# Optimization experiments

Measured on AMD Instinct MI355X. Metric: run time of the kernel, lower is better.

The kernel has to match this reference:

```python
import jax, jax.numpy as jnp
import numpy as np

G, N, C_IN, C_OUT, HEADS = 64, 2048, 64, 64, 2
E = 1_000_000
T = G * N  # total flattened nodes
NEG_SLOPE = 0.2  # PyG GATv2Conv default


def setup_inputs() -> dict:
    key = jax.random.key(0)
    k_x, k_e, k_wl, k_wr, k_a, k_b = jax.random.split(key, 6)
    x = jax.random.normal(k_x, (G, N, C_IN), dtype=jnp.float32)
    edge_index = jax.random.randint(k_e, (2, E), 0, T, dtype=jnp.int64)
    # GATv2Conv params (share_weights=False): separate lin_l / lin_r, per-head att vector, bias
    s = 1.0 / np.sqrt(C_IN)
    W_l = jax.random.uniform(k_wl, (C_IN, HEADS * C_OUT), minval=-s, maxval=s, dtype=jnp.float32)
    W_r = jax.random.uniform(k_wr, (C_IN, HEADS * C_OUT), minval=-s, maxval=s, dtype=jnp.float32)
    att = jax.random.normal(k_a, (HEADS, C_OUT), dtype=jnp.float32) * 0.1
    bias = jax.random.normal(k_b, (HEADS * C_OUT,), dtype=jnp.float32) * 0.01
    return {"x": x, "edge_index": edge_index, "W_l": W_l, "W_r": W_r, "att": att, "bias": bias}


def reference(x, edge_index, W_l, W_r, att, bias):
    # Flatten batched nodes: (G, N, C_in) -> (T, C_in)
    x_flat = x.reshape(-1, C_IN)
    # Linear projections per side, split heads: (T, H, C)
    xl = (x_flat @ W_l).reshape(T, HEADS, C_OUT)
    xr = (x_flat @ W_r).reshape(T, HEADS, C_OUT)
    # add_self_loops=True: append (i, i) for every flattened node
    loop = jnp.arange(T, dtype=edge_index.dtype)
    src = jnp.concatenate([edge_index[0], loop])
    dst = jnp.concatenate([edge_index[1], loop])
    # GATv2 scoring: e_ij = att . LeakyReLU(xl[j] + xr[i])  -> (E', H)
    h = jax.nn.leaky_relu(xl[src] + xr[dst], negative_slope=NEG_SLOPE)
    score = jnp.einsum('ehc,hc->eh', h, att)
    # Segment softmax over incoming edges of each destination node
    m = jax.ops.segment_max(score, dst, num_segments=T)  # (T, H)
    ealpha = jnp.exp(score - m[dst])
    denom = jax.ops.segment_sum(ealpha, dst, num_segments=T)
    alpha = ealpha / denom[dst]  # self-loops guarantee denom > 0
    # Scatter-aggregate messages: out[i] = sum_j alpha_ij * xl[j]
    out = jax.ops.segment_sum(alpha[:, :, None] * xl[src], dst, num_segments=T)  # (T, H, C)
    out = out.reshape(T, HEADS * C_OUT) + bias
    return out.reshape(G, N, HEADS * C_OUT)
```

## Files before the change

kernel.cpp:

```cpp
#include <hip/hip_runtime.h>
#include <hip/hip_bf16.h>

#define T_NODES (64 * 2048)
#define CIN 64
#define HC 128
#define NEG_SLOPE 0.2f
#define GEMM_BLOCKS (T_NODES / 64)

typedef unsigned short ushort_t;
typedef __attribute__((ext_vector_type(8))) short bf16x8;
typedef __attribute__((ext_vector_type(4))) float f32x4;
typedef __attribute__((ext_vector_type(2))) float f32x2;

__device__ __forceinline__ ushort_t f2bf(float x) {
    unsigned u = __float_as_uint(x);
    u += 0x7fffu + ((u >> 16) & 1u);
    return (ushort_t)(u >> 16);
}
__device__ __forceinline__ float bf2f(ushort_t b) {
    return __uint_as_float(((unsigned)b) << 16);
}
__device__ __forceinline__ f32x2 bf2x2(unsigned w) {
    f32x2 r;
    r.x = __uint_as_float(w << 16);
    r.y = __uint_as_float(w & 0xffff0000u);
    return r;
}
__device__ __forceinline__ f32x2 pkmax(f32x2 a, f32x2 b) {
    f32x2 r; r.x = fmaxf(a.x, b.x); r.y = fmaxf(a.y, b.y); return r;
}

__global__ __launch_bounds__(256) void prep_init(const float* __restrict__ Wl,
                                                 const float* __restrict__ Wr,
                                                 uint4* __restrict__ wt,
                                                 unsigned* __restrict__ counts,
                                                 unsigned* __restrict__ partials) {
    const int bid = blockIdx.x, tid = threadIdx.x;
    if (bid < 8) {
        const int t = bid * 256 + tid;
        const int n = t & 255, cc = t >> 8;
        const float* Wsrc = ((n < HC) ? Wl : Wr) + (n & (HC - 1));
        union { ushort_t u[8]; uint4 v; } pk;
#pragma unroll
        for (int j = 0; j < 8; ++j) pk.u[j] = f2bf(Wsrc[(cc * 8 + j) * HC]);
        const int sw = (n & 7) << 4;
        *(uint4*)((char*)wt + n * 128 + ((cc * 16) ^ sw)) = pk.v;
        if (bid == 0 && tid < 128) partials[tid] = 0u;
    } else {
        const int i = (bid - 8) * 256 + tid;
        uint4* c4 = (uint4*)counts;
        c4[i * 2]     = (uint4){0, 0, 0, 0};
        c4[i * 2 + 1] = (uint4){0, 0, 0, 0};
    }
}

__global__ __launch_bounds__(256) void gemm_hist(const float* __restrict__ x,
                                                 const uint4* __restrict__ wt,
                                                 ushort_t* __restrict__ xl,
                                                 ushort_t* __restrict__ xr,
                                                 const int* __restrict__ ei,
                                                 unsigned* __restrict__ counts,
                                                 ushort_t* __restrict__ rank,
                                                 int E, int ET, int histBlocks) {
    __shared__ uint4 lds4[512];
    const int tid = threadIdx.x;

    if (blockIdx.x < histBlocks) {
        const int b = blockIdx.x;
#pragma unroll
        for (int e = 0; e < 4; ++e) {
            int i = b * 1024 + e * 256 + tid;
            if (i < ET) {
                int dst = (i < E) ? ei[E + i] : (i - E);
                rank[i] = (ushort_t)atomicAdd(&counts[dst], 1u);
            }
        }
        return;
    }

    char* abase = (char*)lds4;
    const int row0 = (blockIdx.x - histBlocks) * 64;

    {
        const int r = tid >> 2, c4 = tid & 3;
        const float4* xp = (const float4*)(x + (size_t)(row0 + r) * CIN + c4 * 16);
        float4 f0 = xp[0], f1 = xp[1], f2 = xp[2], f3 = xp[3];
        union { ushort_t u[16]; uint4 v[2]; } pk;
        const float s[16] = {f0.x,f0.y,f0.z,f0.w, f1.x,f1.y,f1.z,f1.w,
                             f2.x,f2.y,f2.z,f2.w, f3.x,f3.y,f3.z,f3.w};
#pragma unroll
        for (int j = 0; j < 16; ++j) pk.u[j] = f2bf(s[j]);
        const int sw = (r & 7) << 4;
        *(uint4*)(abase + r * 128 + ((c4 * 32)      ^ sw)) = pk.v[0];
        *(uint4*)(abase + r * 128 + ((c4 * 32 + 16) ^ sw)) = pk.v[1];
    }
    __syncthreads();

    const int wave = tid >> 6;
    const int lane = tid & 63;
    const int ar = lane & 15;
    const int kb = lane >> 4;
    const char* wb = (const char*)wt;

    bf16x8 afr[2][4], bfr[2][4];
#pragma unroll
    for (int kk = 0; kk < 2; ++kk) {
#pragma unroll
        for (int rt = 0; rt < 4; ++rt) {
            const int r = rt * 16 + ar;
            afr[kk][rt] = *(bf16x8*)(abase + r * 128 + ((kk * 64 + kb * 16) ^ ((r & 7) << 4)));
        }
#pragma unroll
        for (int ct = 0; ct < 4; ++ct) {
            const int n = wave * 64 + ct * 16 + ar;
            bfr[kk][ct] = *(const bf16x8*)(wb + n * 128 + ((kk * 64 + kb * 16) ^ ((n & 7) << 4)));
        }
    }

    f32x4 acc[4][4];
#pragma unroll
    for (int rt = 0; rt < 4; ++rt)
#pragma unroll
        for (int ct = 0; ct < 4; ++ct) acc[rt][ct] = (f32x4){0.f, 0.f, 0.f, 0.f};

#pragma unroll
    for (int kk = 0; kk < 2; ++kk)
#pragma unroll
        for (int rt = 0; rt < 4; ++rt)
#pragma unroll
            for (int ct = 0; ct < 4; ++ct)
                acc[rt][ct] = __builtin_amdgcn_mfma_f32_16x16x32_bf16(
                    afr[kk][rt], bfr[kk][ct], acc[rt][ct], 0, 0, 0);

    ushort_t* op = (wave < 2) ? xl : xr;
    const int colbase = (wave & 1) * 64 + ar;
    const int rowoff = (lane >> 4) * 4;
#pragma unroll
    for (int rt = 0; rt < 4; ++rt)
#pragma unroll
        for (int ct = 0; ct < 4; ++ct)
#pragma unroll
            for (int j = 0; j < 4; ++j)
                op[(size_t)(row0 + rt * 16 + rowoff + j) * HC + colbase + ct * 16] =
                    f2bf(acc[rt][ct][j]);
}

__global__ __launch_bounds__(256) void scan_all(const unsigned* __restrict__ counts,
                                                unsigned* __restrict__ offs,
                                                unsigned* __restrict__ partials) {
    __shared__ unsigned s[256];
    __shared__ unsigned wsum[4];
    const int b = blockIdx.x, t = threadIdx.x;
    const int base_i = b * 1024 + t * 4;
    uint4 c = *(const uint4*)(counts + base_i);
    unsigned mysum = c.x + c.y + c.z + c.w;
    s[t] = mysum;
    __syncthreads();
    for (int off = 1; off < 256; off <<= 1) {
        unsigned v = (t >= off) ? s[t - off] : 0u;
        __syncthreads();
        s[t] += v;
        __syncthreads();
    }
    const unsigned excl = s[t] - mysum;
    if (t == 255)
        __hip_atomic_store(&partials[b], s[255] | 0x80000000u,
                           __ATOMIC_RELEASE, __HIP_MEMORY_SCOPE_AGENT);
    unsigned bs = 0;
    if (t < b) {
        unsigned v;
        do {
            v = __hip_atomic_load(&partials[t], __ATOMIC_ACQUIRE,
                                  __HIP_MEMORY_SCOPE_AGENT);
        } while (!(v & 0x80000000u));
        bs = v & 0x7fffffffu;
    }
#pragma unroll
    for (int off = 32; off; off >>= 1) bs += __shfl_xor(bs, off);
    if ((t & 63) == 0) wsum[t >> 6] = bs;
    __syncthreads();
    const unsigned base = wsum[0] + wsum[1] + wsum[2] + wsum[3];
    uint4 o;
    o.x = excl + base;
    o.y = o.x + c.x;
    o.z = o.y + c.y;
    o.w = o.z + c.z;
    *(uint4*)(offs + base_i) = o;
}

__global__ void scatter_edges(const int* __restrict__ ei,
                              const unsigned* __restrict__ offs,
                              const ushort_t* __restrict__ rank,
                              int* __restrict__ sorted_src, int E, int ET) {
    int i = blockIdx.x * 256 + threadIdx.x;
    if (i >= ET) return;
    int src, dst;
    if (i < E) { src = ei[i]; dst = ei[E + i]; }
    else       { src = dst = i - E; }
    sorted_src[offs[dst] + rank[i]] = src;
}

__global__ __launch_bounds__(256) void fused_aggr(const ushort_t* __restrict__ xl,
                                                  const ushort_t* __restrict__ xr,
                                                  const int* __restrict__ sorted_src,
                                                  const unsigned* __restrict__ offs,
                                                  const unsigned* __restrict__ counts,
                                                  const float* __restrict__ att,
                                                  const float* __restrict__ bias,
                                                  float* __restrict__ out) {
    const int tid = threadIdx.x;
    const int lane = tid & 63;
    int node = (blockIdx.x * 256 + tid) >> 6;
    node = __builtin_amdgcn_readfirstlane(node);
    const int slot = lane >> 4;
    const int sub  = lane & 15;
    const unsigned cb2 = (unsigned)sub * 16u;

    f32x2 attv[4], xrv[4];
    {
        const f32x2* ap = (const f32x2*)(att + sub * 8);
#pragma unroll
        for (int q = 0; q < 4; ++q) attv[q] = ap[q];
        const uint4 xv = *(const uint4*)((const char*)xr + (((unsigned)node << 8) + cb2));
        const unsigned* xw = (const unsigned*)&xv;
#pragma unroll
        for (int q = 0; q < 4; ++q) xrv[q] = bf2x2(xw[q]);
    }

    const int start = (int)offs[node];
    const int cnt   = (int)counts[node];
    const int rounds = (cnt + 3) >> 2;

    f32x2 acc2[4];
#pragma unroll
    for (int q = 0; q < 4; ++q) acc2[q] = (f32x2){0.f, 0.f};
    float d = 0.f;

    for (int r = 0; r < rounds; ++r) {
        const int k = r * 4 + slot;
        const bool valid = k < cnt;
        const int src = sorted_src[start + (valid ? k : 0)];
        const uint4 v = *(const uint4*)((const char*)xl + (((unsigned)src << 8) + cb2));
        const unsigned* vw = (const unsigned*)&v;
        f32x2 a2[4];
        f32x2 p2 = (f32x2){0.f, 0.f};
#pragma unroll
        for (int q = 0; q < 4; ++q) {
            a2[q] = bf2x2(vw[q]);
            f32x2 z = a2[q] + xrv[q];
            z = pkmax(z, z * NEG_SLOPE);
            p2 += attv[q] * z;
        }
        float p = p2.x + p2.y;
        p += __shfl_xor(p, 1);
        p += __shfl_xor(p, 2);
        p += __shfl_xor(p, 4);
        const float e = valid ? __expf(p) : 0.f;
        d += e;
        const f32x2 ev = (f32x2){e, e};
#pragma unroll
        for (int q = 0; q < 4; ++q) acc2[q] += ev * a2[q];
    }

#pragma unroll
    for (int off = 16; off <= 32; off <<= 1) {
        d += __shfl_xor(d, off);
#pragma unroll
        for (int q = 0; q < 4; ++q) {
            acc2[q].x += __shfl_xor(acc2[q].x, off);
            acc2[q].y += __shfl_xor(acc2[q].y, off);
        }
    }

    if (slot == 0) {
        const float inv = 1.f / d;
        const f32x2* bp = (const f32x2*)(bias + sub * 8);
        float4 o0, o1;
        o0.x = acc2[0].x * inv + bp[0].x; o0.y = acc2[0].y * inv + bp[0].y;
        o0.z = acc2[1].x * inv + bp[1].x; o0.w = acc2[1].y * inv + bp[1].y;
        o1.x = acc2[2].x * inv + bp[2].x; o1.y = acc2[2].y * inv + bp[2].y;
        o1.z = acc2[3].x * inv + bp[3].x; o1.w = acc2[3].y * inv + bp[3].y;
        float* op = out + (size_t)node * HC + sub * 8;
        *(float4*)op = o0;
        *(float4*)(op + 4) = o1;
    }
}

extern "C" void kernel_launch(void* const* d_in, const int* in_sizes, int n_in,
                              void* d_out, int out_size, void* d_ws, size_t ws_size,
                              hipStream_t stream) {
    const float* x    = (const float*)d_in[0];
    const int*   ei   = (const int*)d_in[1];
    const float* Wl   = (const float*)d_in[2];
    const float* Wr   = (const float*)d_in[3];
    const float* att  = (const float*)d_in[4];
    const float* bias = (const float*)d_in[5];
    float* out = (float*)d_out;

    const int E  = in_sizes[1] / 2;
    const int ET = E + T_NODES;

    ushort_t* xl = (ushort_t*)d_ws;
    ushort_t* xr = xl + (size_t)T_NODES * HC;
    int* sorted_src = (int*)(xr + (size_t)T_NODES * HC);
    unsigned* counts   = (unsigned*)(sorted_src + ET);
    unsigned* offs     = counts + T_NODES;
    unsigned* partials = offs + T_NODES;
    ushort_t* rank     = (ushort_t*)(partials + 128);
    uint4* wt          = (uint4*)(rank + ((ET + 7) & ~7));

    prep_init<<<72, 256, 0, stream>>>(Wl, Wr, wt, counts, partials);

    const int histBlocks = (ET + 1023) / 1024;
    gemm_hist<<<histBlocks + GEMM_BLOCKS, 256, 0, stream>>>(x, wt, xl, xr,
                                                            ei, counts, rank,
                                                            E, ET, histBlocks);

    scan_all<<<T_NODES / 1024, 256, 0, stream>>>(counts, offs, partials);
    int eblocks = (ET + 255) / 256;
    scatter_edges<<<eblocks, 256, 0, stream>>>(ei, offs, rank, sorted_src, E, ET);

    fused_aggr<<<T_NODES / 4, 256, 0, stream>>>(xl, xr, sorted_src, offs, counts,
                                                att, bias, out);
}
```

Measured before the change: 165.6 us.

## Split projection GEMM across histogram and scatter kernels for load balance

Moves the GEMM tile body into a shared device function and splits the node projection in two. The first half of the row tiles runs alongside the degree histogram, and the second half runs alongside the edge scatter. The aim is to hide GEMM work behind the two atomic- and memory-bound edge passes and even out per-kernel load. The scatter kernel now allocates 8KB of LDS in every block, including scatter-only blocks, which may slightly reduce occupancy.

```diff
diff --git a/kernel.cpp b/kernel.cpp
--- a/kernel.cpp
+++ b/kernel.cpp
@@ -6,6 +6,7 @@
 #define HC 128
 #define NEG_SLOPE 0.2f
 #define GEMM_BLOCKS (T_NODES / 64)
+#define GEMM_HALF (GEMM_BLOCKS / 2)
 
 typedef unsigned short ushort_t;
 typedef __attribute__((ext_vector_type(8))) short bf16x8;
@@ -28,6 +29,77 @@
 }
 __device__ __forceinline__ f32x2 pkmax(f32x2 a, f32x2 b) {
     f32x2 r; r.x = fmaxf(a.x, b.x); r.y = fmaxf(a.y, b.y); return r;
+}
+
+__device__ __forceinline__ void gemm_tile(const float* __restrict__ x,
+                                          const uint4* __restrict__ wt,
+                                          ushort_t* __restrict__ xl,
+                                          ushort_t* __restrict__ xr,
+                                          int row0, int tid, uint4* lds4) {
+    char* abase = (char*)lds4;
+
+    {
+        const int r = tid >> 2, c4 = tid & 3;
+        const float4* xp = (const float4*)(x + (size_t)(row0 + r) * CIN + c4 * 16);
+        float4 f0 = xp[0], f1 = xp[1], f2 = xp[2], f3 = xp[3];
+        union { ushort_t u[16]; uint4 v[2]; } pk;
+        const float s[16] = {f0.x,f0.y,f0.z,f0.w, f1.x,f1.y,f1.z,f1.w,
+                             f2.x,f2.y,f2.z,f2.w, f3.x,f3.y,f3.z,f3.w};
+#pragma unroll
+        for (int j = 0; j < 16; ++j) pk.u[j] = f2bf(s[j]);
+        const int sw = (r & 7) << 4;
+        *(uint4*)(abase + r * 128 + ((c4 * 32)      ^ sw)) = pk.v[0];
+        *(uint4*)(abase + r * 128 + ((c4 * 32 + 16) ^ sw)) = pk.v[1];
+    }
+    __syncthreads();
+
+    const int wave = tid >> 6;
+    const int lane = tid & 63;
+    const int ar = lane & 15;
+    const int kb = lane >> 4;
+    const char* wb = (const char*)wt;
+
+    bf16x8 afr[2][4], bfr[2][4];
+#pragma unroll
+    for (int kk = 0; kk < 2; ++kk) {
+#pragma unroll
+        for (int rt = 0; rt < 4; ++rt) {
+            const int r = rt * 16 + ar;
+            afr[kk][rt] = *(bf16x8*)(abase + r * 128 + ((kk * 64 + kb * 16) ^ ((r & 7) << 4)));
+        }
+#pragma unroll
+        for (int ct = 0; ct < 4; ++ct) {
+            const int n = wave * 64 + ct * 16 + ar;
+            bfr[kk][ct] = *(const bf16x8*)(wb + n * 128 + ((kk * 64 + kb * 16) ^ ((n & 7) << 4)));
+        }
+    }
+
+    f32x4 acc[4][4];
+#pragma unroll
+    for (int rt = 0; rt < 4; ++rt)
+#pragma unroll
+        for (int ct = 0; ct < 4; ++ct) acc[rt][ct] = (f32x4){0.f, 0.f, 0.f, 0.f};
+
+#pragma unroll
+    for (int kk = 0; kk < 2; ++kk)
+#pragma unroll
+        for (int rt = 0; rt < 4; ++rt)
+#pragma unroll
+            for (int ct = 0; ct < 4; ++ct)
+                acc[rt][ct] = __builtin_amdgcn_mfma_f32_16x16x32_bf16(
+                    afr[kk][rt], bfr[kk][ct], acc[rt][ct], 0, 0, 0);
+
+    ushort_t* op = (wave < 2) ? xl : xr;
+    const int colbase = (wave & 1) * 64 + ar;
+    const int rowoff = kb * 4;
+#pragma unroll
+    for (int rt = 0; rt < 4; ++rt)
+#pragma unroll
+        for (int ct = 0; ct < 4; ++ct)
+#pragma unroll
+            for (int j = 0; j < 4; ++j)
+                op[(size_t)(row0 + rt * 16 + rowoff + j) * HC + colbase + ct * 16] =
+                    f2bf(acc[rt][ct][j]);
 }
 
 __global__ __launch_bounds__(256) void prep_init(const float* __restrict__ Wl,
@@ -77,72 +149,7 @@
         }
         return;
     }
-
-    char* abase = (char*)lds4;
-    const int row0 = (blockIdx.x - histBlocks) * 64;
-
-    {
-        const int r = tid >> 2, c4 = tid & 3;
-        const float4* xp = (const float4*)(x + (size_t)(row0 + r) * CIN + c4 * 16);
-        float4 f0 = xp[0], f1 = xp[1], f2 = xp[2], f3 = xp[3];
-        union { ushort_t u[16]; uint4 v[2]; } pk;
-        const float s[16] = {f0.x,f0.y,f0.z,f0.w, f1.x,f1.y,f1.z,f1.w,
-                             f2.x,f2.y,f2.z,f2.w, f3.x,f3.y,f3.z,f3.w};
-#pragma unroll
-        for (int j = 0; j < 16; ++j) pk.u[j] = f2bf(s[j]);
-        const int sw = (r & 7) << 4;
-        *(uint4*)(abase + r * 128 + ((c4 * 32)      ^ sw)) = pk.v[0];
-        *(uint4*)(abase + r * 128 + ((c4 * 32 + 16) ^ sw)) = pk.v[1];
-    }
-    __syncthreads();
-
-    const int wave = tid >> 6;
-    const int lane = tid & 63;
-    const int ar = lane & 15;
-    const int kb = lane >> 4;
-    const char* wb = (const char*)wt;
-
-    bf16x8 afr[2][4], bfr[2][4];
-#pragma unroll
-    for (int kk = 0; kk < 2; ++kk) {
-#pragma unroll
-        for (int rt = 0; rt < 4; ++rt) {
-            const int r = rt * 16 + ar;
-            afr[kk][rt] = *(bf16x8*)(abase + r * 128 + ((kk * 64 + kb * 16) ^ ((r & 7) << 4)));
-        }
-#pragma unroll
-        for (int ct = 0; ct < 4; ++ct) {
-            const int n = wave * 64 + ct * 16 + ar;
-            bfr[kk][ct] = *(const bf16x8*)(wb + n * 128 + ((kk * 64 + kb * 16) ^ ((n & 7) << 4)));
-        }
-    }
-
-    f32x4 acc[4][4];
-#pragma unroll
-    for (int rt = 0; rt < 4; ++rt)
-#pragma unroll
-        for (int ct = 0; ct < 4; ++ct) acc[rt][ct] = (f32x4){0.f, 0.f, 0.f, 0.f};
-
-#pragma unroll
-    for (int kk = 0; kk < 2; ++kk)
-#pragma unroll
-        for (int rt = 0; rt < 4; ++rt)
-#pragma unroll
-            for (int ct = 0; ct < 4; ++ct)
-                acc[rt][ct] = __builtin_amdgcn_mfma_f32_16x16x32_bf16(
-                    afr[kk][rt], bfr[kk][ct], acc[rt][ct], 0, 0, 0);
-
-    ushort_t* op = (wave < 2) ? xl : xr;
-    const int colbase = (wave & 1) * 64 + ar;
-    const int rowoff = (lane >> 4) * 4;
-#pragma unroll
-    for (int rt = 0; rt < 4; ++rt)
-#pragma unroll
-        for (int ct = 0; ct < 4; ++ct)
-#pragma unroll
-            for (int j = 0; j < 4; ++j)
-                op[(size_t)(row0 + rt * 16 + rowoff + j) * HC + colbase + ct * 16] =
-                    f2bf(acc[rt][ct][j]);
+    gemm_tile(x, wt, xl, xr, (blockIdx.x - histBlocks) * 64, tid, lds4);
 }
 
 __global__ __launch_bounds__(256) void scan_all(const unsigned* __restrict__ counts,
@@ -188,16 +195,29 @@
     *(uint4*)(offs + base_i) = o;
 }
 
-__global__ void scatter_edges(const int* __restrict__ ei,
-                              const unsigned* __restrict__ offs,
-                              const ushort_t* __restrict__ rank,
-                              int* __restrict__ sorted_src, int E, int ET) {
-    int i = blockIdx.x * 256 + threadIdx.x;
-    if (i >= ET) return;
-    int src, dst;
-    if (i < E) { src = ei[i]; dst = ei[E + i]; }
-    else       { src = dst = i - E; }
-    sorted_src[offs[dst] + rank[i]] = src;
+__global__ __launch_bounds__(256) void scatter_gemm(const int* __restrict__ ei,
+                                                    const unsigned* __restrict__ offs,
+                                                    const ushort_t* __restrict__ rank,
+                                                    int* __restrict__ sorted_src,
+                                                    const float* __restrict__ x,
+                                                    const uint4* __restrict__ wt,
+                                                    ushort_t* __restrict__ xl,
+                                                    ushort_t* __restrict__ xr,
+                                                    int E, int ET, int sBlocks) {
+    __shared__ uint4 lds4[512];
+    const int tid = threadIdx.x;
+
+    if (blockIdx.x < sBlocks) {
+        int i = blockIdx.x * 256 + tid;
+        if (i < ET) {
+            int src, dst;
+            if (i < E) { src = ei[i]; dst = ei[E + i]; }
+            else       { src = dst = i - E; }
+            sorted_src[offs[dst] + rank[i]] = src;
+        }
+        return;
+    }
+    gemm_tile(x, wt, xl, xr, (T_NODES / 2) + (blockIdx.x - sBlocks) * 64, tid, lds4);
 }
 
 __global__ __launch_bounds__(256) void fused_aggr(const ushort_t* __restrict__ xl,
@@ -312,13 +332,15 @@
     prep_init<<<72, 256, 0, stream>>>(Wl, Wr, wt, counts, partials);
 
     const int histBlocks = (ET + 1023) / 1024;
-    gemm_hist<<<histBlocks + GEMM_BLOCKS, 256, 0, stream>>>(x, wt, xl, xr,
-                                                            ei, counts, rank,
-                                                            E, ET, histBlocks);
+    gemm_hist<<<histBlocks + GEMM_HALF, 256, 0, stream>>>(x, wt, xl, xr,
+                                                          ei, counts, rank,
+                                                          E, ET, histBlocks);
 
     scan_all<<<T_NODES / 1024, 256, 0, stream>>>(counts, offs, partials);
-    int eblocks = (ET + 255) / 256;
-    scatter_edges<<<eblocks, 256, 0, stream>>>(ei, offs, rank, sorted_src, E, ET);
+
+    const int sBlocks = (ET + 255) / 256;
+    scatter_gemm<<<sBlocks + GEMM_HALF, 256, 0, stream>>>(ei, offs, rank, sorted_src,
+                                                          x, wt, xl, xr, E, ET, sBlocks);
 
     fused_aggr<<<T_NODES / 4, 256, 0, stream>>>(xl, xr, sorted_src, offs, counts,
                                                 att, bias, out);
```

Measured after the change: 168.1 us. Within noise of the previous version (+1.5%).
